# Kernel optimization log

Hardware: AMD Instinct MI355X
Metric: run time of the kernel (lower is better)

The kernel has to match this reference:

```python
import jax, jax.numpy as jnp
import numpy as np

B, H, W, C, E, TOP_K = 16, 64, 64, 384, 5, 2


def setup_inputs() -> dict:
    key = jax.random.key(0)
    k1, k2, k3 = jax.random.split(key, 3)
    x = jax.random.normal(k1, (B, H, W, C), dtype=jnp.float32)
    Wg = jax.random.normal(k2, (C, E), dtype=jnp.float32) * 0.02   # router
    We = jax.random.normal(k3, (E, C, C), dtype=jnp.float32) * 0.02  # expert weights
    be = jnp.zeros((E, C), dtype=jnp.float32)                       # expert biases
    return {"x": x, "Wg": Wg, "We": We, "be": be}


def reference(x, Wg, We, be):
    Bx, Hx, Wx, Cx = x.shape
    Ex = Wg.shape[1]
    t = x.reshape(-1, Cx)                      # [N, C] tokens
    N = t.shape[0]

    # --- top-k routing ---
    logits = t @ Wg                            # [N, E]
    top_vals, top_idx = jax.lax.top_k(logits, TOP_K)   # [N, 2]
    gates = jax.nn.softmax(top_vals, axis=-1)          # softmax over selected experts
    combine = jnp.zeros((N, Ex), dtype=t.dtype)
    combine = combine.at[jnp.arange(N)[:, None], top_idx].set(gates)  # [N, E] sparse combine weights

    # --- expert computation (dense over experts, combined with sparse gates) ---
    expert_out = jnp.einsum('nc,ecd->ned', t, We) + be[None]  # [N, E, C]
    y = jnp.einsum('ne,ned->nd', combine, expert_out)         # [N, C]

    # --- LeakyReLU (default slope 0.01); dropout is identity in eval mode ---
    y = jax.nn.leaky_relu(y, negative_slope=0.01)
    return y.reshape(Bx, Hx, Wx, Cx)
```

## Files before the change

kernel.cpp:

```cpp
#include <hip/hip_runtime.h>
#include <stdint.h>

#define TOKENS 65536
#define CDIM 384
#define NEXP 5
#define NPAIR 10
#define CAP 8192
#define NBLK 1024
#define WE_STRIDE (CDIM * CDIM)

typedef __attribute__((ext_vector_type(8))) short short8;
typedef __attribute__((ext_vector_type(4))) float floatx4;

__constant__ int PAIR_A[NPAIR] = {0, 0, 0, 0, 1, 1, 1, 2, 2, 3};
__constant__ int PAIR_B[NPAIR] = {1, 2, 3, 4, 2, 3, 4, 3, 4, 4};

__device__ inline unsigned short f2bf(float f) {
    union { float f; uint32_t u; } v; v.f = f;
    uint32_t r = v.u + 0x7fffu + ((v.u >> 16) & 1u);
    return (unsigned short)(r >> 16);
}

__device__ inline void load_lds16(const void* g, void* l) {
    __builtin_amdgcn_global_load_lds((const __attribute__((address_space(1))) void*)g,
                                     (__attribute__((address_space(3))) void*)l, 16, 0, 0);
}

__global__ __launch_bounds__(256) void router_kernel(const float* __restrict__ x,
                                                     const float* __restrict__ Wg,
                                                     int* __restrict__ blkcnt,
                                                     int* __restrict__ tmeta,
                                                     float2* __restrict__ tgate) {
    __shared__ __align__(16) float  xs[64 * 129];
    __shared__ __align__(16) float  wgs[CDIM * 8];
    __shared__ __align__(16) double part[4 * 64 * NEXP];
    __shared__ __align__(16) double lg[64 * NEXP];
    int t = threadIdx.x, lane = t & 63, w = t >> 6;
    int tok0 = blockIdx.x * 64;

    for (int i = t; i < CDIM * NEXP; i += 256) wgs[(i / NEXP) * 8 + (i % NEXP)] = Wg[i];

    int lrow = t >> 5, loff = (t & 31) * 4;
    double p0 = 0, p1 = 0, p2 = 0, p3 = 0, p4 = 0;
    #pragma unroll
    for (int ch = 0; ch < 3; ++ch) {
        __syncthreads();
        #pragma unroll
        for (int r8 = 0; r8 < 8; ++r8) {
            int row = r8 * 8 + lrow;
            float4 v = *(const float4*)&x[(size_t)(tok0 + row) * CDIM + ch * 128 + loff];
            float* d = &xs[row * 129 + loff];
            d[0] = v.x; d[1] = v.y; d[2] = v.z; d[3] = v.w;
        }
        __syncthreads();
        const float* xr = &xs[lane * 129 + w * 32];
        #pragma unroll
        for (int j = 0; j < 32; ++j) {
            int c = ch * 128 + w * 32 + j;
            float4 w03 = *(const float4*)&wgs[c * 8];
            float  w4  = wgs[c * 8 + 4];
            double xd = (double)xr[j];
            p0 += xd * w03.x; p1 += xd * w03.y; p2 += xd * w03.z;
            p3 += xd * w03.w; p4 += xd * w4;
        }
    }
    double* pr = &part[(w * 64 + lane) * NEXP];
    pr[0] = p0; pr[1] = p1; pr[2] = p2; pr[3] = p3; pr[4] = p4;
    __syncthreads();

    for (int item = t; item < 64 * NEXP; item += 256) {
        lg[item] = part[item] + part[320 + item] + part[640 + item] + part[960 + item];
    }
    __syncthreads();

    if (t < 64) {
        double pa[NEXP];
        #pragma unroll
        for (int e = 0; e < NEXP; ++e) pa[e] = lg[t * NEXP + e];
        int i0 = 0; double m0v = pa[0];
        #pragma unroll
        for (int e = 1; e < NEXP; ++e) if (pa[e] > m0v) { m0v = pa[e]; i0 = e; }
        int i1 = -1; double m1v = -1e300;
        #pragma unroll
        for (int e = 0; e < NEXP; ++e) if (e != i0 && pa[e] > m1v) { m1v = pa[e]; i1 = e; }
        float d  = (float)(m1v - m0v);
        float e1 = expf(d);
        float inv = 1.0f / (1.0f + e1);

        int a  = i0 < i1 ? i0 : i1;
        int b2 = i0 < i1 ? i1 : i0;
        int p  = a * 4 - ((a * (a - 1)) >> 1) + (b2 - a - 1);
        float ga = (a == i0) ? inv : e1 * inv;
        float gb = (a == i0) ? e1 * inv : inv;

        unsigned long long below = (1ull << lane) - 1ull;
        int myrank = 0, myh = 0;
        #pragma unroll
        for (int e = 0; e < NPAIR; ++e) {
            unsigned long long mask = __ballot(p == e);
            if (p == e)    myrank = (int)__popcll(mask & below);
            if (lane == e) myh    = (int)__popcll(mask);
        }
        tmeta[tok0 + lane] = p | (myrank << 8);
        tgate[tok0 + lane] = make_float2(ga, gb);
        if (lane < NPAIR) blkcnt[lane * NBLK + blockIdx.x] = myh;
    }
}

__global__ __launch_bounds__(256) void scan_kernel(const int* __restrict__ blkcnt,
                                                   int* __restrict__ bbase,
                                                   int* __restrict__ cnt) {
    __shared__ int wsum[4];
    int p = blockIdx.x, t = threadIdx.x, lane = t & 63, w = t >> 6;
    int4 v = ((const int4*)(blkcnt + p * NBLK))[t];
    int s0 = v.x, s1 = s0 + v.y, s2 = s1 + v.z, s3 = s2 + v.w;
    int ws = s3;
    #pragma unroll
    for (int d = 1; d < 64; d <<= 1) {
        int o = __shfl_up(ws, d);
        if (lane >= d) ws += o;
    }
    if (lane == 63) wsum[w] = ws;
    __syncthreads();
    int woff = 0;
    for (int k = 0; k < w; ++k) woff += wsum[k];
    int excl = woff + ws - s3;
    int4 b; b.x = excl; b.y = excl + s0; b.z = excl + s1; b.w = excl + s2;
    ((int4*)(bbase + p * NBLK))[t] = b;
    if (t == 255) cnt[p] = excl + s3;
}

__global__ __launch_bounds__(256) void scatter_kernel(const int* __restrict__ tmeta,
                                                      const int* __restrict__ bbase,
                                                      int* __restrict__ bidx) {
    int tok = blockIdx.x * 256 + threadIdx.x;
    int meta = tmeta[tok];
    int p = meta & 255, rank = meta >> 8;
    int pos = bbase[p * NBLK + (tok >> 6)] + rank;
    if (pos < CAP) bidx[p * CAP + pos] = tok;
}

__global__ __launch_bounds__(256) void convert_we(const float* __restrict__ We,
                                                  unsigned short* __restrict__ WeT) {
    __shared__ float tile[64][65];
    int e  = blockIdx.z;
    int c0 = blockIdx.x * 64, d0 = blockIdx.y * 64;
    int t  = threadIdx.x;
    const float* src = We + (size_t)e * WE_STRIDE;
    int dr = t & 15, cr = t >> 4;
    for (int s = 0; s < 64; s += 16) {
        float4 v = *(const float4*)&src[(size_t)(c0 + cr + s) * CDIM + d0 + dr * 4];
        tile[cr + s][dr * 4 + 0] = v.x;
        tile[cr + s][dr * 4 + 1] = v.y;
        tile[cr + s][dr * 4 + 2] = v.z;
        tile[cr + s][dr * 4 + 3] = v.w;
    }
    __syncthreads();
    unsigned short* dst = WeT + (size_t)e * WE_STRIDE;
    int c4 = t & 15, drow = t >> 4;
    for (int s = 0; s < 64; s += 16) {
        int d = drow + s;
        ushort4 o;
        o.x = f2bf(tile[c4 * 4 + 0][d]);
        o.y = f2bf(tile[c4 * 4 + 1][d]);
        o.z = f2bf(tile[c4 * 4 + 2][d]);
        o.w = f2bf(tile[c4 * 4 + 3][d]);
        *(ushort4*)&dst[(size_t)(d0 + d) * CDIM + c0 + c4 * 4] = o;
    }
}

__global__ __launch_bounds__(512, 4) void moe_kernel(const float* __restrict__ x,
                                                     const unsigned short* __restrict__ WeT,
                                                     const int* __restrict__ cnt,
                                                     const int* __restrict__ bidx,
                                                     const float2* __restrict__ tgate,
                                                     const float* __restrict__ be,
                                                     float* __restrict__ out) {
    int bh  = blockIdx.x;
    int bid = (bh & 7) * 240 + (bh >> 3);
    int pq  = bid / 3;
    int nt  = bid - pq * 3;
    int p   = pq >> 6;
    int mt  = pq & 63;

    int nct = cnt[p];
    int m0  = mt * 128;
    if (m0 >= nct) return;
    int valid = nct - m0; if (valid > 128) valid = 128;

    int ea = PAIR_A[p], eb = PAIR_B[p];
    int n0 = nt * 128;
    int t = threadIdx.x, lane = t & 63, wid = t >> 6;
    int wm = wid >> 1, wn = wid & 1;
    int q = lane >> 4, cc = lane & 15;

    __shared__ __align__(16) unsigned short S[4096 * 8];

    floatx4 acc[2][2][4];
    #pragma unroll
    for (int e = 0; e < 2; ++e)
        #pragma unroll
        for (int i = 0; i < 2; ++i)
            #pragma unroll
            for (int j = 0; j < 4; ++j)
                acc[e][i][j] = (floatx4){0.0f, 0.0f, 0.0f, 0.0f};

    int rrow = t >> 2, gp = t & 3;
    int gl = (gp - (rrow >> 1)) & 3;
    const unsigned short* bsrcA = WeT + (size_t)ea * WE_STRIDE + (size_t)(n0 + rrow) * CDIM + gl * 8;
    const unsigned short* bsrcB = WeT + (size_t)eb * WE_STRIDE + (size_t)(n0 + rrow) * CDIM + gl * 8;
    int bdstA = wid * 64;
    int bdstB = 512 + wid * 64;

    int srow = t >> 2, sp = t & 3;
    int arow = m0 + (srow < valid ? srow : valid - 1);
    int gi = bidx[p * CAP + arow];
    const float* xrow = x + (size_t)gi * CDIM + sp * 8;
    int agr = 4 * srow + ((sp + (srow >> 1)) & 3);

    int perm = (q + (cc >> 1)) & 3;
    int a_gr = 4 * (wm * 32 + cc) + perm;
    int b_gr = 4 * (wn * 64 + cc) + perm;

    float4 xreg[2][2];
    xreg[0][0] = *(const float4*)(xrow);
    xreg[0][1] = *(const float4*)(xrow + 4);
    xreg[1][0] = *(const float4*)(xrow + 32);
    xreg[1][1] = *(const float4*)(xrow + 36);
    load_lds16(bsrcA,      S + (size_t)(1024 + bdstA) * 8);
    load_lds16(bsrcB,      S + (size_t)(1024 + bdstB) * 8);
    load_lds16(bsrcA + 32, S + (size_t)(2048 + bdstA) * 8);
    load_lds16(bsrcB + 32, S + (size_t)(2048 + bdstB) * 8);

    #pragma unroll
    for (int kc = 0; kc < 12; ++kc) {
        int buf = kc & 1;
        int bb  = kc - (kc / 3) * 3;
        float4 a0 = xreg[buf][0], a1 = xreg[buf][1];
        short8 av;
        av[0] = f2bf(a0.x); av[1] = f2bf(a0.y); av[2] = f2bf(a0.z); av[3] = f2bf(a0.w);
        av[4] = f2bf(a1.x); av[5] = f2bf(a1.y); av[6] = f2bf(a1.z); av[7] = f2bf(a1.w);
        *(short8*)&S[(size_t)(buf * 512 + agr) * 8] = av;

        if (kc == 0 || kc == 11) {
            asm volatile("s_waitcnt vmcnt(0) lgkmcnt(0)" ::: "memory");
        } else {
            asm volatile("s_waitcnt vmcnt(4) lgkmcnt(0)" ::: "memory");
        }
        __builtin_amdgcn_s_barrier();
        __builtin_amdgcn_sched_barrier(0);

        if (kc < 10) {
            int k2 = (kc + 2) * 32;
            int nb = (kc + 2) % 3;
            xreg[buf][0] = *(const float4*)(xrow + k2);
            xreg[buf][1] = *(const float4*)(xrow + k2 + 4);
            load_lds16(bsrcA + k2, S + (size_t)(1024 + nb * 1024 + bdstA) * 8);
            load_lds16(bsrcB + k2, S + (size_t)(1024 + nb * 1024 + bdstB) * 8);
        }

        int ao = buf * 512, bo = 1024 + bb * 1024;
        short8 af0 = *(const short8*)&S[(size_t)(ao + a_gr) * 8];
        short8 af1 = *(const short8*)&S[(size_t)(ao + a_gr + 64) * 8];
        #pragma unroll
        for (int e = 0; e < 2; ++e) {
            #pragma unroll
            for (int j = 0; j < 4; ++j) {
                short8 bf = *(const short8*)&S[(size_t)(bo + b_gr + e * 512 + j * 64) * 8];
                acc[e][0][j] = __builtin_amdgcn_mfma_f32_16x16x32_bf16(af0, bf, acc[e][0][j], 0, 0, 0);
                acc[e][1][j] = __builtin_amdgcn_mfma_f32_16x16x32_bf16(af1, bf, acc[e][1][j], 0, 0, 0);
            }
        }
    }

    __syncthreads();
    float2* Gp = (float2*)S;
    int*    Ip = (int*)((char*)S + 1024);
    if (t < 128) {
        int rr = m0 + (t < valid ? t : valid - 1);
        int gid = bidx[p * CAP + rr];
        Ip[t] = gid;
        Gp[t] = tgate[gid];
    }
    float ba_[4], bb_[4];
    #pragma unroll
    for (int j = 0; j < 4; ++j) {
        int oc = n0 + wn * 64 + j * 16 + cc;
        ba_[j] = be[ea * CDIM + oc];
        bb_[j] = be[eb * CDIM + oc];
    }
    __syncthreads();

    #pragma unroll
    for (int i = 0; i < 2; ++i) {
        #pragma unroll
        for (int rr4 = 0; rr4 < 4; ++rr4) {
            int trow = wm * 32 + i * 16 + q * 4 + rr4;
            if (trow < valid) {
                float2 g = Gp[trow];
                int gid  = Ip[trow];
                #pragma unroll
                for (int j = 0; j < 4; ++j) {
                    int oc = n0 + wn * 64 + j * 16 + cc;
                    float v = g.x * (acc[0][i][j][rr4] + ba_[j])
                            + g.y * (acc[1][i][j][rr4] + bb_[j]);
                    v = v > 0.0f ? v : 0.01f * v;
                    out[(size_t)gid * CDIM + oc] = v;
                }
            }
        }
    }
}

extern "C" void kernel_launch(void* const* d_in, const int* in_sizes, int n_in,
                              void* d_out, int out_size, void* d_ws, size_t ws_size,
                              hipStream_t stream) {
    const float* x  = (const float*)d_in[0];
    const float* Wg = (const float*)d_in[1];
    const float* We = (const float*)d_in[2];
    const float* be = (const float*)d_in[3];
    float* out = (float*)d_out;

    char* ws = (char*)d_ws;
    int*            cnt    = (int*)ws;
    int*            bidx   = (int*)(ws + 256);
    int*            blkcnt = (int*)(ws + 327936);
    int*            bbase  = (int*)(ws + 368896);
    int*            tmeta  = (int*)(ws + 409856);
    float2*         tgate  = (float2*)(ws + 672000);
    unsigned short* WeT    = (unsigned short*)(ws + 1196288);

    router_kernel<<<NBLK, 256, 0, stream>>>(x, Wg, blkcnt, tmeta, tgate);
    scan_kernel<<<NPAIR, 256, 0, stream>>>(blkcnt, bbase, cnt);
    scatter_kernel<<<TOKENS / 256, 256, 0, stream>>>(tmeta, bbase, bidx);
    convert_we<<<dim3(6, 6, 5), 256, 0, stream>>>(We, WeT);
    moe_kernel<<<NPAIR * 64 * 3, 512, 0, stream>>>(x, WeT, cnt, bidx, tgate, be, out);
}
```

Measured before the change: 246.9 us.

## Fuse scan, scatter and weight conversion into one kernel; raise MFMA wave priority

Merges the per-pair prefix scan, the token scatter and the expert-weight bf16 transpose into a single launch. Each scatter block recomputes its own prefix by reducing all earlier block counts, and the extra blocks do the weight conversion. This removes two kernel launches and their serialization gaps, at the cost of redundant reduction work (up to 10x1024 reads per block) and ten barriers per block. It also wraps the MFMA inner loop in s_setprio to favour waves issuing matrix ops.

```diff
diff --git a/kernel.cpp b/kernel.cpp
--- a/kernel.cpp
+++ b/kernel.cpp
@@ -107,66 +107,73 @@
     }
 }
 
-__global__ __launch_bounds__(256) void scan_kernel(const int* __restrict__ blkcnt,
-                                                   int* __restrict__ bbase,
-                                                   int* __restrict__ cnt) {
-    __shared__ int wsum[4];
-    int p = blockIdx.x, t = threadIdx.x, lane = t & 63, w = t >> 6;
-    int4 v = ((const int4*)(blkcnt + p * NBLK))[t];
-    int s0 = v.x, s1 = s0 + v.y, s2 = s1 + v.z, s3 = s2 + v.w;
-    int ws = s3;
-    #pragma unroll
-    for (int d = 1; d < 64; d <<= 1) {
-        int o = __shfl_up(ws, d);
-        if (lane >= d) ws += o;
-    }
-    if (lane == 63) wsum[w] = ws;
-    __syncthreads();
-    int woff = 0;
-    for (int k = 0; k < w; ++k) woff += wsum[k];
-    int excl = woff + ws - s3;
-    int4 b; b.x = excl; b.y = excl + s0; b.z = excl + s1; b.w = excl + s2;
-    ((int4*)(bbase + p * NBLK))[t] = b;
-    if (t == 255) cnt[p] = excl + s3;
-}
-
-__global__ __launch_bounds__(256) void scatter_kernel(const int* __restrict__ tmeta,
-                                                      const int* __restrict__ bbase,
-                                                      int* __restrict__ bidx) {
-    int tok = blockIdx.x * 256 + threadIdx.x;
-    int meta = tmeta[tok];
-    int p = meta & 255, rank = meta >> 8;
-    int pos = bbase[p * NBLK + (tok >> 6)] + rank;
-    if (pos < CAP) bidx[p * CAP + pos] = tok;
-}
-
-__global__ __launch_bounds__(256) void convert_we(const float* __restrict__ We,
+__global__ __launch_bounds__(256) void mid_kernel(const int* __restrict__ blkcnt,
+                                                  const int* __restrict__ tmeta,
+                                                  int* __restrict__ bidx,
+                                                  int* __restrict__ cnt,
+                                                  const float* __restrict__ We,
                                                   unsigned short* __restrict__ WeT) {
     __shared__ float tile[64][65];
-    int e  = blockIdx.z;
-    int c0 = blockIdx.x * 64, d0 = blockIdx.y * 64;
-    int t  = threadIdx.x;
-    const float* src = We + (size_t)e * WE_STRIDE;
-    int dr = t & 15, cr = t >> 4;
-    for (int s = 0; s < 64; s += 16) {
-        float4 v = *(const float4*)&src[(size_t)(c0 + cr + s) * CDIM + d0 + dr * 4];
-        tile[cr + s][dr * 4 + 0] = v.x;
-        tile[cr + s][dr * 4 + 1] = v.y;
-        tile[cr + s][dr * 4 + 2] = v.z;
-        tile[cr + s][dr * 4 + 3] = v.w;
-    }
-    __syncthreads();
-    unsigned short* dst = WeT + (size_t)e * WE_STRIDE;
-    int c4 = t & 15, drow = t >> 4;
-    for (int s = 0; s < 64; s += 16) {
-        int d = drow + s;
-        ushort4 o;
-        o.x = f2bf(tile[c4 * 4 + 0][d]);
-        o.y = f2bf(tile[c4 * 4 + 1][d]);
-        o.z = f2bf(tile[c4 * 4 + 2][d]);
-        o.w = f2bf(tile[c4 * 4 + 3][d]);
-        *(ushort4*)&dst[(size_t)(d0 + d) * CDIM + c0 + c4 * 4] = o;
-    }
+    __shared__ int   sbase[NPAIR][4];
+    __shared__ int   rred[4];
+    int bid = blockIdx.x;
+    int t = threadIdx.x;
+
+    if (bid >= 256) {
+        int idx = bid - 256;
+        int e   = idx / 36, rem = idx % 36;
+        int c0  = (rem / 6) * 64, d0 = (rem % 6) * 64;
+        const float* src = We + (size_t)e * WE_STRIDE;
+        int dr = t & 15, cr = t >> 4;
+        for (int s = 0; s < 64; s += 16) {
+            float4 v = *(const float4*)&src[(size_t)(c0 + cr + s) * CDIM + d0 + dr * 4];
+            tile[cr + s][dr * 4 + 0] = v.x;
+            tile[cr + s][dr * 4 + 1] = v.y;
+            tile[cr + s][dr * 4 + 2] = v.z;
+            tile[cr + s][dr * 4 + 3] = v.w;
+        }
+        __syncthreads();
+        unsigned short* dst = WeT + (size_t)e * WE_STRIDE;
+        int c4 = t & 15, drow = t >> 4;
+        for (int s = 0; s < 64; s += 16) {
+            int d = drow + s;
+            ushort4 o;
+            o.x = f2bf(tile[c4 * 4 + 0][d]);
+            o.y = f2bf(tile[c4 * 4 + 1][d]);
+            o.z = f2bf(tile[c4 * 4 + 2][d]);
+            o.w = f2bf(tile[c4 * 4 + 3][d]);
+            *(ushort4*)&dst[(size_t)(d0 + d) * CDIM + c0 + c4 * 4] = o;
+        }
+        return;
+    }
+
+    int lane = t & 63, w = t >> 6;
+    int nb4 = bid * 4;
+    for (int p = 0; p < NPAIR; ++p) {
+        int s = 0;
+        for (int j = t; j < nb4; j += 256) s += blkcnt[p * NBLK + j];
+        #pragma unroll
+        for (int d = 1; d < 64; d <<= 1) s += __shfl_xor(s, d);
+        if (lane == 0) rred[w] = s;
+        __syncthreads();
+        if (t == 0) {
+            int S  = rred[0] + rred[1] + rred[2] + rred[3];
+            int c0_ = blkcnt[p * NBLK + nb4 + 0];
+            int c1_ = blkcnt[p * NBLK + nb4 + 1];
+            int c2_ = blkcnt[p * NBLK + nb4 + 2];
+            sbase[p][0] = S;
+            sbase[p][1] = S + c0_;
+            sbase[p][2] = S + c0_ + c1_;
+            sbase[p][3] = S + c0_ + c1_ + c2_;
+            if (bid == 255) cnt[p] = S + c0_ + c1_ + c2_ + blkcnt[p * NBLK + nb4 + 3];
+        }
+        __syncthreads();
+    }
+    int tok  = bid * 256 + t;
+    int meta = tmeta[tok];
+    int p    = meta & 255, rank = meta >> 8;
+    int pos  = sbase[p][t >> 6] + rank;
+    if (pos < CAP) bidx[p * CAP + pos] = tok;
 }
 
 __global__ __launch_bounds__(512, 4) void moe_kernel(const float* __restrict__ x,
@@ -262,6 +269,7 @@
         int ao = buf * 512, bo = 1024 + bb * 1024;
         short8 af0 = *(const short8*)&S[(size_t)(ao + a_gr) * 8];
         short8 af1 = *(const short8*)&S[(size_t)(ao + a_gr + 64) * 8];
+        __builtin_amdgcn_s_setprio(1);
         #pragma unroll
         for (int e = 0; e < 2; ++e) {
             #pragma unroll
@@ -271,6 +279,7 @@
                 acc[e][1][j] = __builtin_amdgcn_mfma_f32_16x16x32_bf16(af1, bf, acc[e][1][j], 0, 0, 0);
             }
         }
+        __builtin_amdgcn_s_setprio(0);
     }
 
     __syncthreads();
@@ -325,14 +334,11 @@
     int*            cnt    = (int*)ws;
     int*            bidx   = (int*)(ws + 256);
     int*            blkcnt = (int*)(ws + 327936);
-    int*            bbase  = (int*)(ws + 368896);
     int*            tmeta  = (int*)(ws + 409856);
     float2*         tgate  = (float2*)(ws + 672000);
     unsigned short* WeT    = (unsigned short*)(ws + 1196288);
 
     router_kernel<<<NBLK, 256, 0, stream>>>(x, Wg, blkcnt, tmeta, tgate);
-    scan_kernel<<<NPAIR, 256, 0, stream>>>(blkcnt, bbase, cnt);
-    scatter_kernel<<<TOKENS / 256, 256, 0, stream>>>(tmeta, bbase, bidx);
-    convert_we<<<dim3(6, 6, 5), 256, 0, stream>>>(We, WeT);
+    mid_kernel<<<436, 256, 0, stream>>>(blkcnt, tmeta, bidx, cnt, We, WeT);
     moe_kernel<<<NPAIR * 64 * 3, 512, 0, stream>>>(x, WeT, cnt, bidx, tgate, be, out);
 }
```

After: 249.7 us. Within noise of the previous version (+1.1%).
